# Performance work log

Measured on AMD Instinct MI355X. Metric: run time of the kernel, lower is better.

## Reference

```python
import jax, jax.numpy as jnp
import numpy as np

D = 1024

def setup_inputs() -> dict:
    key = jax.random.key(0)
    ks = jax.random.split(key, 9)
    s = 1.0 / np.sqrt(D)
    return {
        "x": jax.random.normal(ks[0], (4, 2048, D), dtype=jnp.float32),
        "y": jax.random.normal(ks[1], (4, 2048, D), dtype=jnp.float32),
        "z": jax.random.normal(ks[2], (4, 2048, D), dtype=jnp.float32),
        "Wq": jax.random.uniform(ks[3], (D, D), jnp.float32, -s, s),
        "bq": jax.random.uniform(ks[4], (D,), jnp.float32, -s, s),
        "Wk": jax.random.uniform(ks[5], (D, D), jnp.float32, -s, s),
        "bk": jax.random.uniform(ks[6], (D,), jnp.float32, -s, s),
        "Wv": jax.random.uniform(ks[7], (D, D), jnp.float32, -s, s),
        "bv": jax.random.uniform(ks[8], (D,), jnp.float32, -s, s),
    }

def reference(x, y, z, Wq, bq, Wk, bk, Wv, bv):
    # nn.Linear: x @ W^T + b
    Q = jnp.einsum('bsd,ed->bse', x, Wq) + bq  # [B,S,D]
    K = jnp.einsum('bsd,ed->bse', y, Wk) + bk
    V = jnp.einsum('bsd,ed->bse', z, Wv) + bv
    scores = jnp.einsum('bqd,bkd->bqk', Q, K) / jnp.sqrt(jnp.float32(Q.shape[-1]))
    weights = jax.nn.softmax(scores, axis=-1)  # [B,S,S]
    return jnp.einsum('bqk,bkd->bqd', weights, V)
```

## Files before the change

### kernel.cpp

```cpp
#include <hip/hip_runtime.h>
#include <hip/hip_bf16.h>

typedef unsigned short u16;
typedef __bf16 bf16x8 __attribute__((ext_vector_type(8)));
typedef float  f32x4  __attribute__((ext_vector_type(4)));
typedef u16    u16x8  __attribute__((ext_vector_type(8)));

__device__ __forceinline__ u16 f2bf(float f) {
    unsigned u = __float_as_uint(f);
    u = (u + 0x7fffu + ((u >> 16) & 1u)) >> 16;
    return (u16)u;
}
__device__ __forceinline__ float bf2f(u16 h) {
    return __uint_as_float(((unsigned)h) << 16);
}

__global__ __launch_bounds__(256) void cvt_bf16_kernel(
    const float* __restrict__ src, u16* __restrict__ dst, int n8)
{
    int i = blockIdx.x * 256 + threadIdx.x;
    if (i >= n8) return;
    const float4* s4 = (const float4*)src;
    float4 a = s4[2 * i], b = s4[2 * i + 1];
    u16x8 o;
    o[0] = f2bf(a.x); o[1] = f2bf(a.y); o[2] = f2bf(a.z); o[3] = f2bf(a.w);
    o[4] = f2bf(b.x); o[5] = f2bf(b.y); o[6] = f2bf(b.z); o[7] = f2bf(b.w);
    ((u16x8*)dst)[i] = o;
}

#define BUF_N 24576
#define LDS_N (3 * BUF_N * 2)

__device__ __forceinline__ void gload_lds16(const void* g, void* l) {
    __builtin_amdgcn_global_load_lds(
        (__attribute__((address_space(1))) void*)g,
        (__attribute__((address_space(3))) void*)l, 16, 0, 0);
}

template<bool OUT_BF16, bool HAS_BIAS>
__global__ __launch_bounds__(512, 2) void gemm_p(
    const u16* __restrict__ A, const u16* __restrict__ Bm,
    const float* __restrict__ bias, void* __restrict__ C,
    int M, int N, int K, float scale,
    long long aBS, long long bBS, long long cBS)
{
    extern __shared__ u16 lds[];

    const int gx = gridDim.x, gy = gridDim.y;
    const int slab = gx * gy;
    const int nwg  = slab * gridDim.z;
    const int b    = blockIdx.x + gx * (blockIdx.y + gy * blockIdx.z);
    const int qc   = nwg >> 3;
    const int L    = (b & 7) * qc + (b >> 3);
    const int tz   = L / slab;
    const int rr   = L - tz * slab;
    const int g4   = rr / (gx * 4);
    const int w4   = rr - g4 * (gx * 4);
    const int tx   = w4 >> 2;
    const int ty   = g4 * 4 + (w4 & 3);

    A  += (size_t)tz * aBS;
    Bm += (size_t)tz * bBS;

    const int m0 = ty * 256;
    const int n0 = tx * 128;
    const int tid  = threadIdx.x;
    const int lane = tid & 63;
    const int wave = tid >> 6;
    const int wm   = wave >> 1;
    const int wn   = wave & 1;
    const int fr   = lane & 15;
    const int kg   = lane >> 4;

    const int rl  = tid >> 3;
    const int sw8 = ((tid & 7) ^ (rl & 7)) * 8;
    const u16* gA = A  + (size_t)(m0 + rl) * K + sw8;
    const u16* gB = Bm + (size_t)(n0 + rl) * K + sw8;
    const int ldsW = wave * 512;

    auto stA = [&](u16* bufb, int tk, int c) {
        gload_lds16(gA + (size_t)c * 64 * K + (size_t)tk * 64,
                    bufb + c * 4096 + ldsW);
    };
    auto stB = [&](u16* bufb, int tk, int c) {
        gload_lds16(gB + (size_t)c * 64 * K + (size_t)tk * 64,
                    bufb + 16384 + c * 4096 + ldsW);
    };

    auto rdA = [&](const u16* sa, int m, int ks) {
        return *(const bf16x8*)&sa[(wm * 64 + m * 16 + fr) * 64
                                   + ((((ks << 2) | kg) ^ (fr & 7)) << 3)];
    };
    auto rdB = [&](const u16* sb, int n, int ks) {
        return *(const bf16x8*)&sb[(wn * 64 + n * 16 + fr) * 64
                                   + ((((ks << 2) | kg) ^ (fr & 7)) << 3)];
    };

    f32x4 acc[4][4] = {};
    bf16x8 a0[4], b0[4], a1[4], b1[4];
    const int NT = K / 64;

    u16 *p0 = lds, *p1 = lds + BUF_N, *p2 = lds + 2 * BUF_N;

    #pragma unroll
    for (int c = 0; c < 4; ++c) stA(p0, 0, c);
    #pragma unroll
    for (int c = 0; c < 2; ++c) stB(p0, 0, c);
    #pragma unroll
    for (int c = 0; c < 4; ++c) stA(p1, 1, c);
    #pragma unroll
    for (int c = 0; c < 2; ++c) stB(p1, 1, c);
    asm volatile("s_waitcnt vmcnt(6)" ::: "memory");
    __builtin_amdgcn_s_barrier();

    #pragma unroll
    for (int m = 0; m < 4; ++m) a0[m] = rdA(p0, m, 0);
    #pragma unroll
    for (int n = 0; n < 4; ++n) b0[n] = rdB(p0 + 16384, n, 0);

    for (int t = 0; t < NT; ++t) {
        const u16* sa = p0;
        const u16* sb = p0 + 16384;
        const bool st = (t + 2 < NT);

        #pragma unroll
        for (int m = 0; m < 4; ++m) a1[m] = rdA(sa, m, 1);
        #pragma unroll
        for (int n = 0; n < 4; ++n) b1[n] = rdB(sb, n, 1);
        if (st) {
            #pragma unroll
            for (int c = 0; c < 4; ++c) stA(p2, t + 2, c);
            #pragma unroll
            for (int c = 0; c < 2; ++c) stB(p2, t + 2, c);
        }
        __builtin_amdgcn_s_setprio(1);
        #pragma unroll
        for (int m = 0; m < 4; ++m)
            #pragma unroll
            for (int n = 0; n < 4; ++n)
                acc[m][n] = __builtin_amdgcn_mfma_f32_16x16x32_bf16(
                    a0[m], b0[n], acc[m][n], 0, 0, 0);
        __builtin_amdgcn_s_setprio(0);

        asm volatile("s_waitcnt lgkmcnt(0)" ::: "memory");
        if (st) asm volatile("s_waitcnt vmcnt(6)" ::: "memory");
        else    asm volatile("s_waitcnt vmcnt(0)" ::: "memory");
        __builtin_amdgcn_s_barrier();
        if (t + 1 < NT) {
            const u16* na = p1;
            const u16* nb = p1 + 16384;
            #pragma unroll
            for (int m = 0; m < 4; ++m) a0[m] = rdA(na, m, 0);
            #pragma unroll
            for (int n = 0; n < 4; ++n) b0[n] = rdB(nb, n, 0);
        }
        __builtin_amdgcn_s_setprio(1);
        #pragma unroll
        for (int m = 0; m < 4; ++m)
            #pragma unroll
            for (int n = 0; n < 4; ++n)
                acc[m][n] = __builtin_amdgcn_mfma_f32_16x16x32_bf16(
                    a1[m], b1[n], acc[m][n], 0, 0, 0);
        __builtin_amdgcn_s_setprio(0);

        u16* tmp = p0; p0 = p1; p1 = p2; p2 = tmp;
    }

    if (OUT_BF16) {
        u16* Cb = (u16*)C + (size_t)tz * cBS;
        #pragma unroll
        for (int m = 0; m < 4; ++m) {
            const int row0 = m0 + wm * 64 + m * 16 + kg * 4;
            #pragma unroll
            for (int n = 0; n < 4; ++n) {
                const int col = n0 + wn * 64 + n * 16 + fr;
                const float badd = HAS_BIAS ? bias[col] : 0.0f;
                f32x4 v = acc[m][n];
                #pragma unroll
                for (int q = 0; q < 4; ++q)
                    Cb[(size_t)(row0 + q) * N + col] = f2bf(v[q] * scale + badd);
            }
        }
    } else {
        float* Cf = (float*)C + (size_t)tz * cBS;
        #pragma unroll
        for (int m = 0; m < 4; ++m) {
            const int row0 = m0 + wm * 64 + m * 16 + kg * 4;
            #pragma unroll
            for (int n = 0; n < 4; ++n) {
                const int col = n0 + wn * 64 + n * 16 + fr;
                const float badd = HAS_BIAS ? bias[col] : 0.0f;
                f32x4 v = acc[m][n];
                #pragma unroll
                for (int q = 0; q < 4; ++q)
                    Cf[(size_t)(row0 + q) * N + col] = v[q] * scale + badd;
            }
        }
    }
}

__global__ __launch_bounds__(256) void transpose_bf16(
    const u16* __restrict__ V, u16* __restrict__ Vt)
{
    __shared__ u16 tile[64][72];
    const int b  = blockIdx.z;
    const int k0 = blockIdx.y * 64;
    const int d0 = blockIdx.x * 64;
    const int tr = threadIdx.x >> 3;
    const int tc = (threadIdx.x & 7) * 8;

    const u16* src = V + ((size_t)b * 2048 + k0) * 1024 + d0;
    #pragma unroll
    for (int i = 0; i < 2; ++i) {
        int r = tr + i * 32;
        *(u16x8*)&tile[r][tc] = *(const u16x8*)&src[(size_t)r * 1024 + tc];
    }
    __syncthreads();
    u16* dst = Vt + ((size_t)b * 1024 + d0) * 2048 + k0;
    #pragma unroll
    for (int i = 0; i < 2; ++i) {
        int r = tr + i * 32;
        u16x8 o;
        #pragma unroll
        for (int j = 0; j < 8; ++j) o[j] = tile[tc + j][r];
        *(u16x8*)&dst[(size_t)r * 2048 + tc] = o;
    }
}

__global__ __launch_bounds__(256) void softmax_kernel(u16* __restrict__ SP)
{
    const size_t row = blockIdx.x;
    u16x8* rp = (u16x8*)(SP + row * 2048);
    const int tid  = threadIdx.x;
    const int lane = tid & 63;
    const int wv   = tid >> 6;

    u16x8 v = rp[tid];
    float f[8];
    #pragma unroll
    for (int j = 0; j < 8; ++j) f[j] = bf2f(v[j]);

    float m = f[0];
    #pragma unroll
    for (int j = 1; j < 8; ++j) m = fmaxf(m, f[j]);
    #pragma unroll
    for (int o = 32; o; o >>= 1) m = fmaxf(m, __shfl_xor(m, o, 64));

    __shared__ float red[8];
    if (lane == 0) red[wv] = m;
    __syncthreads();
    m = fmaxf(fmaxf(red[0], red[1]), fmaxf(red[2], red[3]));

    float e[8], s = 0.f;
    #pragma unroll
    for (int j = 0; j < 8; ++j) { e[j] = __expf(f[j] - m); s += e[j]; }
    #pragma unroll
    for (int o = 32; o; o >>= 1) s += __shfl_xor(s, o, 64);
    if (lane == 0) red[4 + wv] = s;
    __syncthreads();
    s = (red[4] + red[5]) + (red[6] + red[7]);
    const float inv = 1.0f / s;

    u16x8 o8;
    #pragma unroll
    for (int j = 0; j < 8; ++j) o8[j] = f2bf(e[j] * inv);
    rp[tid] = o8;
}

extern "C" void kernel_launch(void* const* d_in, const int* in_sizes, int n_in,
                              void* d_out, int out_size, void* d_ws, size_t ws_size,
                              hipStream_t stream)
{
    const int Bn = 4, S = 2048, D = 1024;
    const size_t nx = (size_t)Bn * S * D;
    const size_t nw = (size_t)D * D;

    const float* x  = (const float*)d_in[0];
    const float* y  = (const float*)d_in[1];
    const float* z  = (const float*)d_in[2];
    const float* Wq = (const float*)d_in[3];
    const float* bq = (const float*)d_in[4];
    const float* Wk = (const float*)d_in[5];
    const float* bk = (const float*)d_in[6];
    const float* Wv = (const float*)d_in[7];
    const float* bv = (const float*)d_in[8];

    u16* xb  = (u16*)d_ws;
    u16* yb  = xb + nx;
    u16* zb  = yb + nx;
    u16* wqb = zb + nx;
    u16* wkb = wqb + nw;
    u16* wvb = wkb + nw;
    u16* Qb  = wvb + nw;
    u16* Kb  = Qb + nx;
    u16* Vb  = Kb + nx;
    u16* Vt  = Vb + nx;
    u16* Pb  = xb;

    hipFuncSetAttribute((const void*)gemm_p<true,  true >,
                        hipFuncAttributeMaxDynamicSharedMemorySize, LDS_N);
    hipFuncSetAttribute((const void*)gemm_p<true,  false>,
                        hipFuncAttributeMaxDynamicSharedMemorySize, LDS_N);
    hipFuncSetAttribute((const void*)gemm_p<false, false>,
                        hipFuncAttributeMaxDynamicSharedMemorySize, LDS_N);

    const int n8x = (int)(nx / 8), n8w = (int)(nw / 8);
    cvt_bf16_kernel<<<(n8x + 255) / 256, 256, 0, stream>>>(x, xb, n8x);
    cvt_bf16_kernel<<<(n8x + 255) / 256, 256, 0, stream>>>(y, yb, n8x);
    cvt_bf16_kernel<<<(n8x + 255) / 256, 256, 0, stream>>>(z, zb, n8x);
    cvt_bf16_kernel<<<(n8w + 255) / 256, 256, 0, stream>>>(Wq, wqb, n8w);
    cvt_bf16_kernel<<<(n8w + 255) / 256, 256, 0, stream>>>(Wk, wkb, n8w);
    cvt_bf16_kernel<<<(n8w + 255) / 256, 256, 0, stream>>>(Wv, wvb, n8w);

    dim3 gQKV(D / 128, (Bn * S) / 256, 1);
    gemm_p<true, true><<<gQKV, 512, LDS_N, stream>>>(xb, wqb, bq, Qb, Bn * S, D, D, 1.0f, 0, 0, 0);
    gemm_p<true, true><<<gQKV, 512, LDS_N, stream>>>(yb, wkb, bk, Kb, Bn * S, D, D, 1.0f, 0, 0, 0);
    gemm_p<true, true><<<gQKV, 512, LDS_N, stream>>>(zb, wvb, bv, Vb, Bn * S, D, D, 1.0f, 0, 0, 0);

    transpose_bf16<<<dim3(D / 64, S / 64, Bn), 256, 0, stream>>>(Vb, Vt);

    gemm_p<true, false><<<dim3(S / 128, S / 256, Bn), 512, LDS_N, stream>>>(
        Qb, Kb, nullptr, Pb, S, S, D, 0.03125f,
        (long long)S * D, (long long)S * D, (long long)S * S);

    softmax_kernel<<<Bn * S, 256, 0, stream>>>(Pb);

    gemm_p<false, false><<<dim3(D / 128, S / 256, Bn), 512, LDS_N, stream>>>(
        Pb, Vt, nullptr, d_out, S, D, S, 1.0f,
        (long long)S * S, (long long)D * S, (long long)S * D);
}
```

Measured before the change: 322.0 us.

## Shrink GEMM K-tile to 32 for higher occupancy and batch conversion launches

The GEMM K-step per stage drops from 64 to 32, which halves the LDS per stage (three buffers of 12288 u16). It also uses a new swizzle for 32-wide rows and raises launch bounds to 4 workgroups per CU. The two-phase register double-buffered fragment loads are replaced with a single read-then-MFMA step per tile, and there is one barrier per iteration. The goal is more resident waves to hide latency, at the cost of twice as many loop iterations and barriers and less overlap of LDS reads with MFMA. The six conversion launches are also merged into two launches, each using a z-dimension over three tensors.

```diff
diff --git a/kernel.cpp b/kernel.cpp
--- a/kernel.cpp
+++ b/kernel.cpp
@@ -15,21 +15,24 @@
     return __uint_as_float(((unsigned)h) << 16);
 }
 
-__global__ __launch_bounds__(256) void cvt_bf16_kernel(
-    const float* __restrict__ src, u16* __restrict__ dst, int n8)
+__global__ __launch_bounds__(256) void cvt3_bf16_kernel(
+    const float* __restrict__ s0, const float* __restrict__ s1,
+    const float* __restrict__ s2, u16* __restrict__ dst, size_t dstride, int n8)
 {
     int i = blockIdx.x * 256 + threadIdx.x;
     if (i >= n8) return;
+    const float* src = (blockIdx.z == 0) ? s0 : (blockIdx.z == 1) ? s1 : s2;
+    u16* d = dst + (size_t)blockIdx.z * dstride;
     const float4* s4 = (const float4*)src;
     float4 a = s4[2 * i], b = s4[2 * i + 1];
     u16x8 o;
     o[0] = f2bf(a.x); o[1] = f2bf(a.y); o[2] = f2bf(a.z); o[3] = f2bf(a.w);
     o[4] = f2bf(b.x); o[5] = f2bf(b.y); o[6] = f2bf(b.z); o[7] = f2bf(b.w);
-    ((u16x8*)dst)[i] = o;
-}
-
-#define BUF_N 24576
-#define LDS_N (3 * BUF_N * 2)
+    ((u16x8*)d)[i] = o;
+}
+
+#define BUF_U 12288
+#define LDS_B (3 * BUF_U * 2)
 
 __device__ __forceinline__ void gload_lds16(const void* g, void* l) {
     __builtin_amdgcn_global_load_lds(
@@ -37,8 +40,12 @@
         (__attribute__((address_space(3))) void*)l, 16, 0, 0);
 }
 
+__device__ __forceinline__ int swz_g(int r) {
+    return (r & 3) ^ (((r >> 2) & 1) << 1) ^ ((r >> 3) & 1);
+}
+
 template<bool OUT_BF16, bool HAS_BIAS>
-__global__ __launch_bounds__(512, 2) void gemm_p(
+__global__ __launch_bounds__(512, 4) void gemm_k32(
     const u16* __restrict__ A, const u16* __restrict__ Bm,
     const float* __restrict__ bias, void* __restrict__ C,
     int M, int N, int K, float scale,
@@ -72,97 +79,64 @@
     const int fr   = lane & 15;
     const int kg   = lane >> 4;
 
-    const int rl  = tid >> 3;
-    const int sw8 = ((tid & 7) ^ (rl & 7)) * 8;
-    const u16* gA = A  + (size_t)(m0 + rl) * K + sw8;
-    const u16* gB = Bm + (size_t)(n0 + rl) * K + sw8;
-    const int ldsW = wave * 512;
+    const int r_ = tid >> 2;
+    const int s_ = (tid & 3) ^ swz_g(r_);
+    const u16* gA = A  + (size_t)(m0 + r_) * K + s_ * 8;
+    const u16* gB = Bm + (size_t)(n0 + r_) * K + s_ * 8;
+    const int dstW = wave * 512;
 
     auto stA = [&](u16* bufb, int tk, int c) {
-        gload_lds16(gA + (size_t)c * 64 * K + (size_t)tk * 64,
-                    bufb + c * 4096 + ldsW);
+        gload_lds16(gA + (size_t)c * 128 * K + tk * 32, bufb + c * 4096 + dstW);
     };
-    auto stB = [&](u16* bufb, int tk, int c) {
-        gload_lds16(gB + (size_t)c * 64 * K + (size_t)tk * 64,
-                    bufb + 16384 + c * 4096 + ldsW);
+    auto stB = [&](u16* bufb, int tk) {
+        gload_lds16(gB + tk * 32, bufb + 8192 + dstW);
     };
 
-    auto rdA = [&](const u16* sa, int m, int ks) {
-        return *(const bf16x8*)&sa[(wm * 64 + m * 16 + fr) * 64
-                                   + ((((ks << 2) | kg) ^ (fr & 7)) << 3)];
+    auto rdA = [&](const u16* sa, int m) {
+        const int R  = wm * 64 + m * 16 + fr;
+        const int sl = kg ^ swz_g(R);
+        return *(const bf16x8*)&sa[R * 32 + sl * 8];
     };
-    auto rdB = [&](const u16* sb, int n, int ks) {
-        return *(const bf16x8*)&sb[(wn * 64 + n * 16 + fr) * 64
-                                   + ((((ks << 2) | kg) ^ (fr & 7)) << 3)];
+    auto rdB = [&](const u16* sb, int n) {
+        const int R  = wn * 64 + n * 16 + fr;
+        const int sl = kg ^ swz_g(R);
+        return *(const bf16x8*)&sb[R * 32 + sl * 8];
     };
 
     f32x4 acc[4][4] = {};
-    bf16x8 a0[4], b0[4], a1[4], b1[4];
-    const int NT = K / 64;
-
-    u16 *p0 = lds, *p1 = lds + BUF_N, *p2 = lds + 2 * BUF_N;
-
-    #pragma unroll
-    for (int c = 0; c < 4; ++c) stA(p0, 0, c);
-    #pragma unroll
-    for (int c = 0; c < 2; ++c) stB(p0, 0, c);
-    #pragma unroll
-    for (int c = 0; c < 4; ++c) stA(p1, 1, c);
-    #pragma unroll
-    for (int c = 0; c < 2; ++c) stB(p1, 1, c);
-    asm volatile("s_waitcnt vmcnt(6)" ::: "memory");
+    const int NT = K / 32;
+
+    u16 *p0 = lds, *p1 = lds + BUF_U, *p2 = lds + 2 * BUF_U;
+
+    stA(p0, 0, 0); stA(p0, 0, 1); stB(p0, 0);
+    stA(p1, 1, 0); stA(p1, 1, 1); stB(p1, 1);
+    asm volatile("s_waitcnt vmcnt(3)" ::: "memory");
     __builtin_amdgcn_s_barrier();
 
-    #pragma unroll
-    for (int m = 0; m < 4; ++m) a0[m] = rdA(p0, m, 0);
-    #pragma unroll
-    for (int n = 0; n < 4; ++n) b0[n] = rdB(p0 + 16384, n, 0);
-
     for (int t = 0; t < NT; ++t) {
-        const u16* sa = p0;
-        const u16* sb = p0 + 16384;
         const bool st = (t + 2 < NT);
-
-        #pragma unroll
-        for (int m = 0; m < 4; ++m) a1[m] = rdA(sa, m, 1);
-        #pragma unroll
-        for (int n = 0; n < 4; ++n) b1[n] = rdB(sb, n, 1);
-        if (st) {
-            #pragma unroll
-            for (int c = 0; c < 4; ++c) stA(p2, t + 2, c);
-            #pragma unroll
-            for (int c = 0; c < 2; ++c) stB(p2, t + 2, c);
-        }
+        if (st) { stA(p2, t + 2, 0); stA(p2, t + 2, 1); stB(p2, t + 2); }
+
+        bf16x8 a[4], bfr[4];
+        #pragma unroll
+        for (int m = 0; m < 4; ++m) a[m] = rdA(p0, m);
+        #pragma unroll
+        for (int n = 0; n < 4; ++n) bfr[n] = rdB(p0 + 8192, n);
+
         __builtin_amdgcn_s_setprio(1);
         #pragma unroll
         for (int m = 0; m < 4; ++m)
             #pragma unroll
             for (int n = 0; n < 4; ++n)
                 acc[m][n] = __builtin_amdgcn_mfma_f32_16x16x32_bf16(
-                    a0[m], b0[n], acc[m][n], 0, 0, 0);
+                    a[m], bfr[n], acc[m][n], 0, 0, 0);
         __builtin_amdgcn_s_setprio(0);
 
-        asm volatile("s_waitcnt lgkmcnt(0)" ::: "memory");
-        if (st) asm volatile("s_waitcnt vmcnt(6)" ::: "memory");
-        else    asm volatile("s_waitcnt vmcnt(0)" ::: "memory");
-        __builtin_amdgcn_s_barrier();
         if (t + 1 < NT) {
-            const u16* na = p1;
-            const u16* nb = p1 + 16384;
-            #pragma unroll
-            for (int m = 0; m < 4; ++m) a0[m] = rdA(na, m, 0);
-            #pragma unroll
-            for (int n = 0; n < 4; ++n) b0[n] = rdB(nb, n, 0);
+            if (st) asm volatile("s_waitcnt vmcnt(3)" ::: "memory");
+            else    asm volatile("s_waitcnt vmcnt(0)" ::: "memory");
+            __builtin_amdgcn_s_barrier();
         }
-        __builtin_amdgcn_s_setprio(1);
-        #pragma unroll
-        for (int m = 0; m < 4; ++m)
-            #pragma unroll
-            for (int n = 0; n < 4; ++n)
-                acc[m][n] = __builtin_amdgcn_mfma_f32_16x16x32_bf16(
-                    a1[m], b1[n], acc[m][n], 0, 0, 0);
-        __builtin_amdgcn_s_setprio(0);
-
         u16* tmp = p0; p0 = p1; p1 = p2; p2 = tmp;
     }
 
@@ -297,35 +271,33 @@
     u16* Vt  = Vb + nx;
     u16* Pb  = xb;
 
-    hipFuncSetAttribute((const void*)gemm_p<true,  true >,
-                        hipFuncAttributeMaxDynamicSharedMemorySize, LDS_N);
-    hipFuncSetAttribute((const void*)gemm_p<true,  false>,
-                        hipFuncAttributeMaxDynamicSharedMemorySize, LDS_N);
-    hipFuncSetAttribute((const void*)gemm_p<false, false>,
-                        hipFuncAttributeMaxDynamicSharedMemorySize, LDS_N);
+    hipFuncSetAttribute((const void*)gemm_k32<true,  true >,
+                        hipFuncAttributeMaxDynamicSharedMemorySize, LDS_B);
+    hipFuncSetAttribute((const void*)gemm_k32<true,  false>,
+                        hipFuncAttributeMaxDynamicSharedMemorySize, LDS_B);
+    hipFuncSetAttribute((const void*)gemm_k32<false, false>,
+                        hipFuncAttributeMaxDynamicSharedMemorySize, LDS_B);
 
     const int n8x = (int)(nx / 8), n8w = (int)(nw / 8);
-    cvt_bf16_kernel<<<(n8x + 255) / 256, 256, 0, stream>>>(x, xb, n8x);
-    cvt_bf16_kernel<<<(n8x + 255) / 256, 256, 0, stream>>>(y, yb, n8x);
-    cvt_bf16_kernel<<<(n8x + 255) / 256, 256, 0, stream>>>(z, zb, n8x);
-    cvt_bf16_kernel<<<(n8w + 255) / 256, 256, 0, stream>>>(Wq, wqb, n8w);
-    cvt_bf16_kernel<<<(n8w + 255) / 256, 256, 0, stream>>>(Wk, wkb, n8w);
-    cvt_bf16_kernel<<<(n8w + 255) / 256, 256, 0, stream>>>(Wv, wvb, n8w);
+    cvt3_bf16_kernel<<<dim3((n8x + 255) / 256, 1, 3), 256, 0, stream>>>(
+        x, y, z, xb, nx, n8x);
+    cvt3_bf16_kernel<<<dim3((n8w + 255) / 256, 1, 3), 256, 0, stream>>>(
+        Wq, Wk, Wv, wqb, nw, n8w);
 
     dim3 gQKV(D / 128, (Bn * S) / 256, 1);
-    gemm_p<true, true><<<gQKV, 512, LDS_N, stream>>>(xb, wqb, bq, Qb, Bn * S, D, D, 1.0f, 0, 0, 0);
-    gemm_p<true, true><<<gQKV, 512, LDS_N, stream>>>(yb, wkb, bk, Kb, Bn * S, D, D, 1.0f, 0, 0, 0);
-    gemm_p<true, true><<<gQKV, 512, LDS_N, stream>>>(zb, wvb, bv, Vb, Bn * S, D, D, 1.0f, 0, 0, 0);
+    gemm_k32<true, true><<<gQKV, 512, LDS_B, stream>>>(xb, wqb, bq, Qb, Bn * S, D, D, 1.0f, 0, 0, 0);
+    gemm_k32<true, true><<<gQKV, 512, LDS_B, stream>>>(yb, wkb, bk, Kb, Bn * S, D, D, 1.0f, 0, 0, 0);
+    gemm_k32<true, true><<<gQKV, 512, LDS_B, stream>>>(zb, wvb, bv, Vb, Bn * S, D, D, 1.0f, 0, 0, 0);
 
     transpose_bf16<<<dim3(D / 64, S / 64, Bn), 256, 0, stream>>>(Vb, Vt);
 
-    gemm_p<true, false><<<dim3(S / 128, S / 256, Bn), 512, LDS_N, stream>>>(
+    gemm_k32<true, false><<<dim3(S / 128, S / 256, Bn), 512, LDS_B, stream>>>(
         Qb, Kb, nullptr, Pb, S, S, D, 0.03125f,
         (long long)S * D, (long long)S * D, (long long)S * S);
 
     softmax_kernel<<<Bn * S, 256, 0, stream>>>(Pb);
 
-    gemm_p<false, false><<<dim3(D / 128, S / 256, Bn), 512, LDS_N, stream>>>(
+    gemm_k32<false, false><<<dim3(D / 128, S / 256, Bn), 512, LDS_B, stream>>>(
         Pb, Vt, nullptr, d_out, S, D, S, 1.0f,
         (long long)S * S, (long long)D * S, (long long)S * D);
 }
```

Result: slower. 332.0 us (+3.1%).

## Fuse softmax into QK and PV GEMM epilogues and batch QKV projections

Applied to the files above, without the earlier changes.

Removes the standalone softmax kernel. The QK GEMM epilogue now writes exp(score) in bf16 and accumulates per-row sums with atomics, and the PV GEMM divides by those row sums. The three QKV projection GEMMs and the input conversions are merged into single launches indexed by blockIdx.z. Skipping the max subtraction risks overflow for large scores, and the atomic row sums add contention and nondeterminism.

```diff
diff --git a/kernel.cpp b/kernel.cpp
--- a/kernel.cpp
+++ b/kernel.cpp
@@ -11,21 +11,27 @@
     u = (u + 0x7fffu + ((u >> 16) & 1u)) >> 16;
     return (u16)u;
 }
-__device__ __forceinline__ float bf2f(u16 h) {
-    return __uint_as_float(((unsigned)h) << 16);
-}
-
-__global__ __launch_bounds__(256) void cvt_bf16_kernel(
-    const float* __restrict__ src, u16* __restrict__ dst, int n8)
+
+__global__ __launch_bounds__(256) void zero_kernel(float* __restrict__ p, int n)
+{
+    int i = blockIdx.x * 256 + threadIdx.x;
+    if (i < n) p[i] = 0.0f;
+}
+
+__global__ __launch_bounds__(256) void cvt3_bf16_kernel(
+    const float* __restrict__ s0, const float* __restrict__ s1,
+    const float* __restrict__ s2, u16* __restrict__ dst, size_t dstride, int n8)
 {
     int i = blockIdx.x * 256 + threadIdx.x;
     if (i >= n8) return;
+    const float* src = (blockIdx.z == 0) ? s0 : (blockIdx.z == 1) ? s1 : s2;
+    u16* d = dst + (size_t)blockIdx.z * dstride;
     const float4* s4 = (const float4*)src;
     float4 a = s4[2 * i], b = s4[2 * i + 1];
     u16x8 o;
     o[0] = f2bf(a.x); o[1] = f2bf(a.y); o[2] = f2bf(a.z); o[3] = f2bf(a.w);
     o[4] = f2bf(b.x); o[5] = f2bf(b.y); o[6] = f2bf(b.z); o[7] = f2bf(b.w);
-    ((u16x8*)dst)[i] = o;
+    ((u16x8*)d)[i] = o;
 }
 
 #define BUF_N 24576
@@ -37,10 +43,12 @@
         (__attribute__((address_space(3))) void*)l, 16, 0, 0);
 }
 
-template<bool OUT_BF16, bool HAS_BIAS>
+template<int MODE>
 __global__ __launch_bounds__(512, 2) void gemm_p(
     const u16* __restrict__ A, const u16* __restrict__ Bm,
-    const float* __restrict__ bias, void* __restrict__ C,
+    const float* __restrict__ bz0, const float* __restrict__ bz1,
+    const float* __restrict__ bz2, void* __restrict__ C,
+    float* __restrict__ rowsum,
     int M, int N, int K, float scale,
     long long aBS, long long bBS, long long cBS)
 {
@@ -166,7 +174,8 @@
         u16* tmp = p0; p0 = p1; p1 = p2; p2 = tmp;
     }
 
-    if (OUT_BF16) {
+    if constexpr (MODE == 0) {
+        const float* bias = (tz == 0) ? bz0 : (tz == 1) ? bz1 : bz2;
         u16* Cb = (u16*)C + (size_t)tz * cBS;
         #pragma unroll
         for (int m = 0; m < 4; ++m) {
@@ -174,26 +183,70 @@
             #pragma unroll
             for (int n = 0; n < 4; ++n) {
                 const int col = n0 + wn * 64 + n * 16 + fr;
-                const float badd = HAS_BIAS ? bias[col] : 0.0f;
+                const float badd = bias[col];
                 f32x4 v = acc[m][n];
                 #pragma unroll
                 for (int q = 0; q < 4; ++q)
                     Cb[(size_t)(row0 + q) * N + col] = f2bf(v[q] * scale + badd);
             }
         }
+    } else if constexpr (MODE == 1) {
+        u16* Cb = (u16*)C + (size_t)tz * cBS;
+        float rs[4][4];
+        #pragma unroll
+        for (int m = 0; m < 4; ++m)
+            #pragma unroll
+            for (int q = 0; q < 4; ++q) rs[m][q] = 0.0f;
+        #pragma unroll
+        for (int m = 0; m < 4; ++m) {
+            const int row0 = m0 + wm * 64 + m * 16 + kg * 4;
+            #pragma unroll
+            for (int n = 0; n < 4; ++n) {
+                const int col = n0 + wn * 64 + n * 16 + fr;
+                f32x4 v = acc[m][n];
+                #pragma unroll
+                for (int q = 0; q < 4; ++q) {
+                    float e = __expf(v[q] * scale);
+                    rs[m][q] += e;
+                    Cb[(size_t)(row0 + q) * N + col] = f2bf(e);
+                }
+            }
+        }
+        #pragma unroll
+        for (int m = 0; m < 4; ++m)
+            #pragma unroll
+            for (int q = 0; q < 4; ++q) {
+                float v = rs[m][q];
+                v += __shfl_xor(v, 1, 64);
+                v += __shfl_xor(v, 2, 64);
+                v += __shfl_xor(v, 4, 64);
+                v += __shfl_xor(v, 8, 64);
+                rs[m][q] = v;
+            }
+        if (fr == 0) {
+            float* rsb = rowsum + (size_t)tz * M;
+            #pragma unroll
+            for (int m = 0; m < 4; ++m) {
+                const int row0 = m0 + wm * 64 + m * 16 + kg * 4;
+                #pragma unroll
+                for (int q = 0; q < 4; ++q)
+                    atomicAdd(&rsb[row0 + q], rs[m][q]);
+            }
+        }
     } else {
         float* Cf = (float*)C + (size_t)tz * cBS;
+        const float* rsb = rowsum + (size_t)tz * M;
         #pragma unroll
         for (int m = 0; m < 4; ++m) {
             const int row0 = m0 + wm * 64 + m * 16 + kg * 4;
+            const f32x4 s4 = *(const f32x4*)&rsb[row0];
             #pragma unroll
             for (int n = 0; n < 4; ++n) {
                 const int col = n0 + wn * 64 + n * 16 + fr;
-                const float badd = HAS_BIAS ? bias[col] : 0.0f;
                 f32x4 v = acc[m][n];
                 #pragma unroll
                 for (int q = 0; q < 4; ++q)
-                    Cf[(size_t)(row0 + q) * N + col] = v[q] * scale + badd;
+                    Cf[(size_t)(row0 + q) * N + col] = v[q] / s4[q];
             }
         }
     }
@@ -225,46 +278,6 @@
         for (int j = 0; j < 8; ++j) o[j] = tile[tc + j][r];
         *(u16x8*)&dst[(size_t)r * 2048 + tc] = o;
     }
-}
-
-__global__ __launch_bounds__(256) void softmax_kernel(u16* __restrict__ SP)
-{
-    const size_t row = blockIdx.x;
-    u16x8* rp = (u16x8*)(SP + row * 2048);
-    const int tid  = threadIdx.x;
-    const int lane = tid & 63;
-    const int wv   = tid >> 6;
-
-    u16x8 v = rp[tid];
-    float f[8];
-    #pragma unroll
-    for (int j = 0; j < 8; ++j) f[j] = bf2f(v[j]);
-
-    float m = f[0];
-    #pragma unroll
-    for (int j = 1; j < 8; ++j) m = fmaxf(m, f[j]);
-    #pragma unroll
-    for (int o = 32; o; o >>= 1) m = fmaxf(m, __shfl_xor(m, o, 64));
-
-    __shared__ float red[8];
-    if (lane == 0) red[wv] = m;
-    __syncthreads();
-    m = fmaxf(fmaxf(red[0], red[1]), fmaxf(red[2], red[3]));
-
-    float e[8], s = 0.f;
-    #pragma unroll
-    for (int j = 0; j < 8; ++j) { e[j] = __expf(f[j] - m); s += e[j]; }
-    #pragma unroll
-    for (int o = 32; o; o >>= 1) s += __shfl_xor(s, o, 64);
-    if (lane == 0) red[4 + wv] = s;
-    __syncthreads();
-    s = (red[4] + red[5]) + (red[6] + red[7]);
-    const float inv = 1.0f / s;
-
-    u16x8 o8;
-    #pragma unroll
-    for (int j = 0; j < 8; ++j) o8[j] = f2bf(e[j] * inv);
-    rp[tid] = o8;
 }
 
 extern "C" void kernel_launch(void* const* d_in, const int* in_sizes, int n_in,
@@ -286,46 +299,40 @@
     const float* bv = (const float*)d_in[8];
 
     u16* xb  = (u16*)d_ws;
-    u16* yb  = xb + nx;
-    u16* zb  = yb + nx;
-    u16* wqb = zb + nx;
-    u16* wkb = wqb + nw;
-    u16* wvb = wkb + nw;
-    u16* Qb  = wvb + nw;
+    u16* wqb = xb + 3 * nx;
+    u16* Qb  = wqb + 3 * nw;
     u16* Kb  = Qb + nx;
     u16* Vb  = Kb + nx;
     u16* Vt  = Vb + nx;
+    float* sums = (float*)(Vt + nx);
     u16* Pb  = xb;
 
-    hipFuncSetAttribute((const void*)gemm_p<true,  true >,
+    hipFuncSetAttribute((const void*)gemm_p<0>,
                         hipFuncAttributeMaxDynamicSharedMemorySize, LDS_N);
-    hipFuncSetAttribute((const void*)gemm_p<true,  false>,
+    hipFuncSetAttribute((const void*)gemm_p<1>,
                         hipFuncAttributeMaxDynamicSharedMemorySize, LDS_N);
-    hipFuncSetAttribute((const void*)gemm_p<false, false>,
+    hipFuncSetAttribute((const void*)gemm_p<2>,
                         hipFuncAttributeMaxDynamicSharedMemorySize, LDS_N);
 
+    zero_kernel<<<(Bn * S + 255) / 256, 256, 0, stream>>>(sums, Bn * S);
+
     const int n8x = (int)(nx / 8), n8w = (int)(nw / 8);
-    cvt_bf16_kernel<<<(n8x + 255) / 256, 256, 0, stream>>>(x, xb, n8x);
-    cvt_bf16_kernel<<<(n8x + 255) / 256, 256, 0, stream>>>(y, yb, n8x);
-    cvt_bf16_kernel<<<(n8x + 255) / 256, 256, 0, stream>>>(z, zb, n8x);
-    cvt_bf16_kernel<<<(n8w + 255) / 256, 256, 0, stream>>>(Wq, wqb, n8w);
-    cvt_bf16_kernel<<<(n8w + 255) / 256, 256, 0, stream>>>(Wk, wkb, n8w);
-    cvt_bf16_kernel<<<(n8w + 255) / 256, 256, 0, stream>>>(Wv, wvb, n8w);
-
-    dim3 gQKV(D / 128, (Bn * S) / 256, 1);
-    gemm_p<true, true><<<gQKV, 512, LDS_N, stream>>>(xb, wqb, bq, Qb, Bn * S, D, D, 1.0f, 0, 0, 0);
-    gemm_p<true, true><<<gQKV, 512, LDS_N, stream>>>(yb, wkb, bk, Kb, Bn * S, D, D, 1.0f, 0, 0, 0);
-    gemm_p<true, true><<<gQKV, 512, LDS_N, stream>>>(zb, wvb, bv, Vb, Bn * S, D, D, 1.0f, 0, 0, 0);
+    cvt3_bf16_kernel<<<dim3((n8x + 255) / 256, 1, 3), 256, 0, stream>>>(
+        x, y, z, xb, nx, n8x);
+    cvt3_bf16_kernel<<<dim3((n8w + 255) / 256, 1, 3), 256, 0, stream>>>(
+        Wq, Wk, Wv, wqb, nw, n8w);
+
+    gemm_p<0><<<dim3(D / 128, (Bn * S) / 256, 3), 512, LDS_N, stream>>>(
+        xb, wqb, bq, bk, bv, Qb, nullptr, Bn * S, D, D, 1.0f,
+        (long long)nx, (long long)nw, (long long)nx);
 
     transpose_bf16<<<dim3(D / 64, S / 64, Bn), 256, 0, stream>>>(Vb, Vt);
 
-    gemm_p<true, false><<<dim3(S / 128, S / 256, Bn), 512, LDS_N, stream>>>(
-        Qb, Kb, nullptr, Pb, S, S, D, 0.03125f,
+    gemm_p<1><<<dim3(S / 128, S / 256, Bn), 512, LDS_N, stream>>>(
+        Qb, Kb, nullptr, nullptr, nullptr, Pb, sums, S, S, D, 0.03125f,
         (long long)S * D, (long long)S * D, (long long)S * S);
 
-    softmax_kernel<<<Bn * S, 256, 0, stream>>>(Pb);
-
-    gemm_p<false, false><<<dim3(D / 128, S / 256, Bn), 512, LDS_N, stream>>>(
-        Pb, Vt, nullptr, d_out, S, D, S, 1.0f,
+    gemm_p<2><<<dim3(D / 128, S / 256, Bn), 512, LDS_N, stream>>>(
+        Pb, Vt, nullptr, nullptr, nullptr, d_out, sums, S, D, S, 1.0f,
         (long long)S * S, (long long)D * S, (long long)S * D);
 }
```

Result: faster. 301.0 us (-6.5%).
